# Kernel optimization log

Measured on AMD Instinct MI355X. Metric: run time of the kernel, lower is better.

Reference implementation:

```python
import jax, jax.numpy as jnp
import numpy as np

SLOPE = 0.2  # leaky_relu_slope for both LVC block and kernel predictor (passed through)
DILATIONS = (1, 3, 9, 27)
HOP = 256
STRIDE = 8
IN_CH = 32
KSZ = 3  # conv_kernel_size


def conv1d(x, w, b, dilation=1, padding=0):
    # x: (B,C,T), w: (O,I,K) torch layout
    y = jax.lax.conv_general_dilated(
        x, w, window_strides=(1,), padding=[(padding, padding)],
        rhs_dilation=(dilation,), dimension_numbers=('NCH', 'OIH', 'NCH'))
    return y + b[None, :, None]


def conv_transpose1d(x, w, b, stride, padding, output_padding=0):
    # w: torch ConvTranspose1d layout (Cin, Cout, K)
    w_ = jnp.flip(w, -1).transpose(1, 0, 2)  # (Cout, Cin, K)
    K = w.shape[2]
    pad = (K - 1 - padding, K - 1 - padding + output_padding)
    y = jax.lax.conv_general_dilated(
        x, w_, window_strides=(1,), padding=[pad],
        lhs_dilation=(stride,), dimension_numbers=('NCH', 'OIH', 'NCH'))
    return y + b[None, :, None]


def lrelu(x, slope=SLOPE):
    return jnp.where(x >= 0, x, slope * x)


def location_variable_convolution(x, kernel, bias, hop):
    # x: (B,C,T), kernel: (B,C,O,k,L), bias: (B,O,L); T == L*hop; dilation==1 path
    B, C, T = x.shape
    _, _, O, k, L = kernel.shape
    pad = (k - 1) // 2
    xp = jnp.pad(x, ((0, 0), (0, 0), (pad, pad)))
    # gather per-segment sliding windows: (L, hop, k) index into time axis
    idx = (jnp.arange(L)[:, None, None] * hop
           + jnp.arange(hop)[None, :, None]
           + jnp.arange(k)[None, None, :])
    xw = xp[:, :, idx]  # (B, C, L, hop, k)
    o = jnp.einsum('bclsk,bcokl->bols', xw, kernel)  # (B, O, L, hop)
    o = o + bias[:, :, :, None]
    return o.reshape(B, O, L * hop)


def kernel_predictor(spec, kp_in_w, kp_in_b, rb_w1, rb_b1, rb_w2, rb_b2,
                     kern_w, kern_b, bias_w, bias_b):
    B, _, L = spec.shape
    h = conv1d(spec, kp_in_w, kp_in_b, padding=2)  # k=5, pad=2
    for i in range(3):  # num_blocks = 3
        r = h
        h = conv1d(h, rb_w1[i], rb_b1[i], padding=1)
        h = lrelu(h)
        h = conv1d(h, rb_w2[i], rb_b2[i], padding=1)
        h = lrelu(h) + r
    kh = conv1d(h, kern_w, kern_b, padding=1)
    bh = conv1d(h, bias_w, bias_b, padding=1)
    n_layers = len(DILATIONS)
    kernels = kh.reshape(B, n_layers, IN_CH, 2 * IN_CH, KSZ, L)
    biases = bh.reshape(B, n_layers, 2 * IN_CH, L)
    return kernels, biases


def reference(hidden_states, spectrogram, convt_w, convt_b, kp_in_w, kp_in_b,
              rb_w1, rb_b1, rb_w2, rb_b2, kern_w, kern_b, bias_w, bias_b,
              lvc_w, lvc_b):
    h = conv_transpose1d(hidden_states, convt_w, convt_b,
                         stride=STRIDE, padding=STRIDE // 2 + STRIDE % 2,
                         output_padding=STRIDE % 2)
    kernels, biases = kernel_predictor(spectrogram, kp_in_w, kp_in_b,
                                       rb_w1, rb_b1, rb_w2, rb_b2,
                                       kern_w, kern_b, bias_w, bias_b)
    for i, d in enumerate(DILATIONS):
        r = h
        h = lrelu(h)
        h = conv1d(h, lvc_w[i], lvc_b[i], dilation=d, padding=d * (KSZ - 1) // 2)
        h = lrelu(h)
        h = location_variable_convolution(h, kernels[:, i], biases[:, i], HOP)
        h = jax.nn.sigmoid(h[:, :IN_CH, :]) * jnp.tanh(h[:, IN_CH:, :]) + r
    return h


def setup_inputs() -> dict:
    key = jax.random.key(0)
    ks = jax.random.split(key, 12)
    B, COND, L, H = 4, 100, 256, 64
    T = L * HOP  # 65536 output samples
    s = jnp.float32(0.02)
    d = {}
    d['hidden_states'] = jax.random.normal(ks[0], (B, IN_CH, T // STRIDE), jnp.float32)
    d['spectrogram'] = jax.random.normal(ks[1], (B, COND, L), jnp.float32)
    d['convt_w'] = jax.random.normal(ks[2], (IN_CH, IN_CH, 2 * STRIDE), jnp.float32) * s
    d['convt_b'] = jnp.zeros((IN_CH,), jnp.float32)
    d['kp_in_w'] = jax.random.normal(ks[3], (H, COND, 5), jnp.float32) * s
    d['kp_in_b'] = jnp.zeros((H,), jnp.float32)
    d['rb_w1'] = jax.random.normal(ks[4], (3, H, H, 3), jnp.float32) * s
    d['rb_b1'] = jnp.zeros((3, H), jnp.float32)
    d['rb_w2'] = jax.random.normal(ks[5], (3, H, H, 3), jnp.float32) * s
    d['rb_b2'] = jnp.zeros((3, H), jnp.float32)
    KC = IN_CH * 2 * IN_CH * KSZ * len(DILATIONS)  # 24576
    d['kern_w'] = jax.random.normal(ks[6], (KC, H, 3), jnp.float32) * s
    d['kern_b'] = jnp.zeros((KC,), jnp.float32)
    BC = 2 * IN_CH * len(DILATIONS)  # 256
    d['bias_w'] = jax.random.normal(ks[7], (BC, H, 3), jnp.float32) * s
    d['bias_b'] = jnp.zeros((BC,), jnp.float32)
    d['lvc_w'] = jax.random.normal(ks[8], (len(DILATIONS), IN_CH, IN_CH, 3), jnp.float32) * s
    d['lvc_b'] = jnp.zeros((len(DILATIONS), IN_CH), jnp.float32)
    return d
```

## Files before the change

kernel.cpp:

```cpp
#include <hip/hip_runtime.h>
#include <math.h>

#define NB 4
#define T 65536
#define TIN 8192
#define LL 256
#define KCL 6144

__device__ __forceinline__ float lrelu_f(float v) { return v >= 0.f ? v : 0.2f * v; }

__global__ void __launch_bounds__(256) prep1(
    const float* __restrict__ rb_w1, const float* __restrict__ rb_w2,
    const float* __restrict__ kp_in_w,
    float* __restrict__ trb, float* __restrict__ tkpin) {
  __shared__ float t[64][193];
  const int bid = blockIdx.x, tid = threadIdx.x;
  if (bid < 6) {
    int i = bid >> 1, which = bid & 1;
    const float* src = (which ? rb_w2 : rb_w1) + (size_t)i * 12288;
    float* dst = trb + (size_t)bid * 12288;
    for (int idx = tid; idx < 64 * 192; idx += 256) {
      int o = idx / 192, J = idx % 192;
      t[o][J] = src[(size_t)o * 192 + J];
    }
    __syncthreads();
    for (int idx = tid; idx < 64 * 192; idx += 256) {
      int J = idx >> 6, o = idx & 63;
      dst[(size_t)J * 64 + o] = t[o][J];
    }
  } else {
    for (int idx = tid; idx < 500 * 64; idx += 256) {
      int row = idx >> 6, o = idx & 63;
      tkpin[idx] = kp_in_w[o * 500 + row];
    }
  }
}

union Phase1LDS {
  struct { float xs[32][264]; float wm[64][128]; } cvt;
  struct { float hs[4][64][20]; float xsp[4][100][24]; } trk;
};

__global__ void __launch_bounds__(512) phase1(
    const float* __restrict__ x, const float* __restrict__ cw,
    const float* __restrict__ cbias, float* __restrict__ hout,
    const float* __restrict__ spec,
    const float* __restrict__ tkpin, const float* __restrict__ kp_in_b,
    const float* __restrict__ trb, const float* __restrict__ rb_b1,
    const float* __restrict__ rb_b2, float* __restrict__ kp_h) {
  __shared__ Phase1LDS sm;
  const int bid = blockIdx.x;
  const int tid = threadIdx.x;
  const int lane = tid & 63, wv = tid >> 6;

  if (bid < 64) {
    if (wv >= 4) return;
    const int unit = bid * 4 + wv;
    const int b = unit >> 6;
    const int chunk = unit & 63;
    const int l0 = chunk * 4;
    const int og = lane >> 1;
    const int colg = lane & 1;
    const int colg8 = colg * 8;
    const int obase = og * 2;
    float (*hsu)[20] = sm.trk.hs[wv];
    float (*xspu)[24] = sm.trk.xsp[wv];

    for (int i = lane; i < 64 * 20; i += 64) ((float*)hsu)[i] = 0.f;

    for (int i = lane; i < 100 * 24; i += 64) {
      int cin = i / 24, cx = i - cin * 24;
      float v = 0.f;
      if (cx < 20) {
        int labs = l0 - 8 + cx;
        if (labs >= 0 && labs < 256)
          v = spec[((size_t)b * 100 + cin) * LL + labs];
      }
      xspu[cin][cx] = v;
    }

    float hcur[2][8];
    {
      float acc[2][8];
      float2 bb = *(const float2*)(kp_in_b + obase);
#pragma unroll
      for (int q = 0; q < 8; ++q) { acc[0][q] = bb.x; acc[1][q] = bb.y; }
#pragma unroll 2
      for (int cin = 0; cin < 100; ++cin) {
        float x12[12];
        *(float4*)&x12[0] = *(const float4*)&xspu[cin][colg8];
        *(float4*)&x12[4] = *(const float4*)&xspu[cin][colg8 + 4];
        *(float4*)&x12[8] = *(const float4*)&xspu[cin][colg8 + 8];
        const float* wp = tkpin + (size_t)(cin * 5) * 64 + obase;
#pragma unroll
        for (int k = 0; k < 5; ++k) {
          float2 w = *(const float2*)(wp + k * 64);
#pragma unroll
          for (int q = 0; q < 8; ++q) {
            acc[0][q] += x12[q + k] * w.x;
            acc[1][q] += x12[q + k] * w.y;
          }
        }
      }
#pragma unroll
      for (int oi = 0; oi < 2; ++oi)
#pragma unroll
        for (int q = 0; q < 8; ++q) {
          int rel = colg8 + q, labs = l0 - 6 + rel;
          float v = (labs >= 0 && labs < 256) ? acc[oi][q] : 0.f;
          hcur[oi][q] = v;
          hsu[obase + oi][rel + 1] = v;
        }
    }

    for (int cv = 0; cv < 6; ++cv) {
      const float* wb = trb + (size_t)cv * 12288;
      const float* bp = (cv & 1) ? rb_b2 + (cv >> 1) * 64 : rb_b1 + (cv >> 1) * 64;
      float2 bb = *(const float2*)(bp + obase);
      float acc[2][8];
#pragma unroll
      for (int q = 0; q < 8; ++q) { acc[0][q] = bb.x; acc[1][q] = bb.y; }
#pragma unroll 2
      for (int c = 0; c < 64; ++c) {
        float x10[10];
        *(float4*)&x10[0] = *(const float4*)&hsu[c][colg8];
        *(float4*)&x10[4] = *(const float4*)&hsu[c][colg8 + 4];
        *(float2*)&x10[8] = *(const float2*)&hsu[c][colg8 + 8];
        const float* wp = wb + (size_t)(c * 192) + obase;
        float2 w0 = *(const float2*)(wp);
        float2 w1 = *(const float2*)(wp + 64);
        float2 w2 = *(const float2*)(wp + 128);
#pragma unroll
        for (int q = 0; q < 8; ++q) {
          acc[0][q] += x10[q] * w0.x + x10[q + 1] * w1.x + x10[q + 2] * w2.x;
          acc[1][q] += x10[q] * w0.y + x10[q + 1] * w1.y + x10[q + 2] * w2.y;
        }
      }
      const int lo = cv + 1, hi = 15 - cv;
#pragma unroll
      for (int oi = 0; oi < 2; ++oi)
#pragma unroll
        for (int q = 0; q < 8; ++q) {
          int rel = colg8 + q, labs = l0 - 6 + rel;
          float v = lrelu_f(acc[oi][q]);
          if (cv & 1) v += hcur[oi][q];
          bool ok = (rel >= lo) && (rel < hi) && (labs >= 0) && (labs < 256);
          v = ok ? v : 0.f;
          if (cv & 1) hcur[oi][q] = v;
          if (cv < 5) hsu[obase + oi][rel + 1] = v;
        }
    }

#pragma unroll
    for (int oi = 0; oi < 2; ++oi)
#pragma unroll
      for (int q = 0; q < 8; ++q) {
        int rel = colg8 + q;
        if (rel >= 6 && rel < 10)
          kp_h[((size_t)b * 64 + obase + oi) * LL + l0 + rel - 6] = hcur[oi][q];
      }
    return;
  }

  const int cb = bid - 64;
  const int bx = cb % 33;
  const int rr = cb / 33;
  const int mtp = rr & 1;
  const int b = rr >> 1;
  const int s0base = bx * 256;
  float (*xs)[264] = sm.cvt.xs;
  float (*wm)[128] = sm.cvt.wm;

  const float* xb = x + (size_t)b * 32 * TIN;
  for (int idx = tid; idx < 32 * 64; idx += 512) {
    int c = idx >> 6, q = idx & 63;
    int p = s0base + q * 4;
    float4 v = (p + 3 < TIN) ? *(const float4*)(xb + c * TIN + p)
                             : make_float4(0.f, 0.f, 0.f, 0.f);
    *(float4*)&xs[c][4 + 4 * q] = v;
  }
  if (tid < 32) {
    int p = s0base - 1;
    xs[tid][3] = (p >= 0) ? xb[tid * TIN + p] : 0.f;
  }
  for (int idx = tid; idx < 8192; idx += 512) {
    int i = idx >> 7, mm = idx & 127;
    int oo = mtp * 16 + (mm >> 3), k0 = mm & 7;
    wm[i][mm] = (i < 32) ? cw[i * 512 + oo * 16 + k0]
                         : cw[(i - 32) * 512 + oo * 16 + k0 + 8];
  }
  __syncthreads();

  float acc[2][8][4];
#pragma unroll
  for (int ol = 0; ol < 2; ++ol) {
    float bo = cbias[mtp * 16 + wv * 2 + ol];
#pragma unroll
    for (int k0 = 0; k0 < 8; ++k0)
#pragma unroll
      for (int si = 0; si < 4; ++si) acc[ol][k0][si] = bo;
  }

  for (int c = 0; c < 32; ++c) {
    float xm1[4], x0[4];
#pragma unroll
    for (int si = 0; si < 4; ++si) {
      xm1[si] = xs[c][lane + si * 64 + 3];
      x0[si]  = xs[c][lane + si * 64 + 4];
    }
    float w0[16], w1[16];
#pragma unroll
    for (int q = 0; q < 4; ++q) {
      *(float4*)&w0[q * 4] = *(const float4*)&wm[c][wv * 16 + q * 4];
      *(float4*)&w1[q * 4] = *(const float4*)&wm[32 + c][wv * 16 + q * 4];
    }
#pragma unroll
    for (int ol = 0; ol < 2; ++ol)
#pragma unroll
      for (int k0 = 0; k0 < 8; ++k0)
#pragma unroll
        for (int si = 0; si < 4; ++si)
          acc[ol][k0][si] += x0[si] * w0[ol * 8 + k0] + xm1[si] * w1[ol * 8 + k0];
  }

#pragma unroll
  for (int ol = 0; ol < 2; ++ol) {
    float* ob = hout + ((size_t)b * 32 + mtp * 16 + wv * 2 + ol) * T;
#pragma unroll
    for (int si = 0; si < 4; ++si) {
      int tb = (s0base + lane + si * 64) * 8 - 4;
      if (tb >= 0 && tb < T)
        *(float4*)(ob + tb) = make_float4(acc[ol][0][si], acc[ol][1][si],
                                          acc[ol][2][si], acc[ol][3][si]);
      if (tb + 4 >= 0 && tb + 4 < T)
        *(float4*)(ob + tb + 4) = make_float4(acc[ol][4][si], acc[ol][5][si],
                                              acc[ol][6][si], acc[ol][7][si]);
    }
  }
}

__global__ void __launch_bounds__(256, 3) kern_head(const float* __restrict__ kp_h,
                                                    const float* __restrict__ kw,
                                                    const float* __restrict__ kb,
                                                    const float* __restrict__ bias_w,
                                                    const float* __restrict__ bias_b,
                                                    float* __restrict__ kh,
                                                    float* __restrict__ bh, int layer) {
    const int bx = blockIdx.x, b = blockIdx.y;
    const bool isbias = (bx >= 192);
    const int tid = threadIdx.x, lane = tid & 63, wv = tid >> 6;
    __shared__ float xs[32][264];
    __shared__ float ws[96][36];

    int g = 0, oc0 = 0, ci = 0, kk = 0, ocb0 = 0;
    const float* wsrc;
    size_t wrow0;
    int wstride;
    if (!isbias) {
        g = bx >> 1; oc0 = (bx & 1) * 32;
        ci = g / 3; kk = g - ci * 3;
        wsrc = kw + (size_t)layer * KCL * 192;
        wrow0 = (size_t)((ci * 64 + oc0) * 3 + kk) * 192;
        wstride = 576;
    } else {
        ocb0 = (bx - 192) * 32;
        wsrc = bias_w;
        wrow0 = (size_t)ocb0 * 192;
        wstride = 192;
    }

    float acc[8][4];
#pragma unroll
    for (int oi = 0; oi < 8; ++oi) {
        float bv = isbias ? bias_b[ocb0 + wv * 8 + oi]
                          : kb[layer * KCL + (ci * 64 + oc0 + wv * 8 + oi) * 3 + kk];
#pragma unroll
        for (int si = 0; si < 4; ++si) acc[oi][si] = bv;
    }

    for (int half = 0; half < 2; ++half) {
        const int hc0 = half * 32;
        __syncthreads();
        for (int idx = tid; idx < 32 * 64; idx += 256) {
            int c = idx >> 6, q = idx & 63;
            *(float4*)&xs[c][4 + 4 * q] =
                *(const float4*)(kp_h + ((size_t)b * 64 + hc0 + c) * LL + 4 * q);
        }
        if (tid < 32) { xs[tid][3] = 0.f; xs[tid][260] = 0.f; }
        for (int idx = tid; idx < 3072; idx += 256) {
            int ocl = idx / 96, jj = idx - ocl * 96;
            ws[jj][ocl] = wsrc[wrow0 + (size_t)ocl * wstride + hc0 * 3 + jj];
        }
        __syncthreads();
        for (int c = 0; c < 32; ++c) {
#pragma unroll
            for (int t = 0; t < 3; ++t) {
                float wv8[8];
                *(float4*)&wv8[0] = *(const float4*)&ws[c * 3 + t][wv * 8];
                *(float4*)&wv8[4] = *(const float4*)&ws[c * 3 + t][wv * 8 + 4];
                float xv[4];
#pragma unroll
                for (int si = 0; si < 4; ++si) xv[si] = xs[c][lane + si * 64 + t + 3];
#pragma unroll
                for (int oi = 0; oi < 8; ++oi)
#pragma unroll
                    for (int si = 0; si < 4; ++si)
                        acc[oi][si] += wv8[oi] * xv[si];
            }
        }
    }

    if (!isbias) {
#pragma unroll
        for (int si = 0; si < 4; ++si) {
            int l = lane + si * 64;
            float* op = kh + ((size_t)b * LL + l) * KCL + g * 64 + oc0 + wv * 8;
            *(float4*)(op)     = make_float4(acc[0][si], acc[1][si], acc[2][si], acc[3][si]);
            *(float4*)(op + 4) = make_float4(acc[4][si], acc[5][si], acc[6][si], acc[7][si]);
        }
    } else {
#pragma unroll
        for (int oi = 0; oi < 8; ++oi) {
            float* op = bh + ((size_t)b * 256 + ocb0 + wv * 8 + oi) * LL;
#pragma unroll
            for (int si = 0; si < 4; ++si)
                op[lane + si * 64] = acc[oi][si];
        }
    }
}

__global__ void __launch_bounds__(512, 4) layer_fused(
    const float* __restrict__ kh, const float* __restrict__ bh,
    const float* __restrict__ w, const float* __restrict__ bias,
    const float* __restrict__ hin, float* __restrict__ hout,
    int layer, int dil) {
    const int l = blockIdx.x, b = blockIdx.y;
    const int tid = threadIdx.x, lane = tid & 63, wv = tid >> 6;
    const int t0 = l * 256;
    __shared__ float xh[32][316];
    __shared__ float ks[KCL];
    __shared__ float ws[96][36];

    const float* hb = hin + (size_t)b * 32 * T;
    for (int idx = tid; idx < 32 * 64; idx += 512) {
        int c = idx >> 6, q = idx & 63;
        float4 v = *(const float4*)(hb + (size_t)c * T + t0 + 4 * q);
        *(float4*)&xh[c][32 + 4 * q] = make_float4(lrelu_f(v.x), lrelu_f(v.y),
                                                   lrelu_f(v.z), lrelu_f(v.w));
    }
    for (int idx = tid; idx < 32 * 60; idx += 512) {
        int c = idx / 60, r = idx - c * 60;
        int jj = (r < 32) ? r : (256 + r);
        int t = t0 + jj - 32;
        xh[c][jj] = (t >= 0 && t < T) ? lrelu_f(hb[(size_t)c * T + t]) : 0.f;
    }
    {
        const float4* kp = (const float4*)(kh + ((size_t)b * LL + l) * KCL);
        float4* kd = (float4*)ks;
        for (int idx = tid; idx < KCL / 4; idx += 512) kd[idx] = kp[idx];
    }
    for (int idx = tid; idx < 3072; idx += 512) {
        int oc = idx / 96, ck = idx - oc * 96;
        ws[ck][oc] = w[oc * 96 + ck];
    }
    __syncthreads();

    const int oc4 = wv * 4;
    float yv[5][4];
    {
        float a[5][4];
#pragma unroll
        for (int oi = 0; oi < 4; ++oi) {
            float bv = bias[oc4 + oi];
#pragma unroll
            for (int si = 0; si < 5; ++si) a[si][oi] = bv;
        }
        for (int c = 0; c < 32; ++c) {
#pragma unroll
            for (int k = 0; k < 3; ++k) {
                float4 wq = *(const float4*)&ws[c * 3 + k][oc4];
                float xv[5];
#pragma unroll
                for (int si = 0; si < 5; ++si) {
                    int col = lane + si * 64;
                    int colc = (col < 258) ? col : 257;
                    xv[si] = xh[c][colc + 31 + (k - 1) * dil];
                }
#pragma unroll
                for (int si = 0; si < 5; ++si) {
                    a[si][0] += xv[si] * wq.x;
                    a[si][1] += xv[si] * wq.y;
                    a[si][2] += xv[si] * wq.z;
                    a[si][3] += xv[si] * wq.w;
                }
            }
        }
#pragma unroll
        for (int si = 0; si < 5; ++si) {
            int t = t0 - 1 + lane + si * 64;
            bool tval = (t >= 0 && t < T);
#pragma unroll
            for (int oi = 0; oi < 4; ++oi)
                yv[si][oi] = tval ? lrelu_f(a[si][oi]) : 0.f;
        }
    }
    __syncthreads();

#pragma unroll
    for (int si = 0; si < 5; ++si) {
        int col = lane + si * 64;
        if (col < 258) {
#pragma unroll
            for (int oi = 0; oi < 4; ++oi) xh[oc4 + oi][col + 31] = yv[si][oi];
        }
    }
    __syncthreads();

    const int oc8 = (wv & 3) * 8;
    const int sh  = wv >> 2;
    float acc_a[8][2], acc_g[8][2];
#pragma unroll
    for (int oi = 0; oi < 8; ++oi) {
        float ba = bh[((size_t)b * 256 + layer * 64 + oc8 + oi) * LL + l];
        float bg = bh[((size_t)b * 256 + layer * 64 + 32 + oc8 + oi) * LL + l];
#pragma unroll
        for (int si = 0; si < 2; ++si) { acc_a[oi][si] = ba; acc_g[oi][si] = bg; }
    }

    for (int c = 0; c < 32; ++c) {
#pragma unroll
        for (int k = 0; k < 3; ++k) {
            const float* kr = ks + (c * 3 + k) * 64;
            float wa[8], wg[8];
            *(float4*)&wa[0] = *(const float4*)(kr + oc8);
            *(float4*)&wa[4] = *(const float4*)(kr + oc8 + 4);
            *(float4*)&wg[0] = *(const float4*)(kr + 32 + oc8);
            *(float4*)&wg[4] = *(const float4*)(kr + 32 + oc8 + 4);
            float xv2[2];
#pragma unroll
            for (int si = 0; si < 2; ++si) {
                int s = lane + (sh * 2 + si) * 64;
                xv2[si] = xh[c][s + k + 31];
            }
#pragma unroll
            for (int oi = 0; oi < 8; ++oi)
#pragma unroll
                for (int si = 0; si < 2; ++si) {
                    acc_a[oi][si] += wa[oi] * xv2[si];
                    acc_g[oi][si] += wg[oi] * xv2[si];
                }
        }
    }

#pragma unroll
    for (int oi = 0; oi < 8; ++oi) {
        const float* hip = hin + ((size_t)b * 32 + oc8 + oi) * T + t0;
        float* hop = hout + ((size_t)b * 32 + oc8 + oi) * T + t0;
#pragma unroll
        for (int si = 0; si < 2; ++si) {
            int s = lane + (sh * 2 + si) * 64;
            float a = acc_a[oi][si], g = acc_g[oi][si];
            float sg = 1.f / (1.f + __expf(-a));
            float th = tanhf(g);
            hop[s] = sg * th + hip[s];
        }
    }
}

extern "C" void kernel_launch(void* const* d_in, const int* in_sizes, int n_in,
                              void* d_out, int out_size, void* d_ws, size_t ws_size,
                              hipStream_t stream) {
    const float* hidden  = (const float*)d_in[0];
    const float* spec    = (const float*)d_in[1];
    const float* convt_w = (const float*)d_in[2];
    const float* convt_b = (const float*)d_in[3];
    const float* kp_in_w = (const float*)d_in[4];
    const float* kp_in_b = (const float*)d_in[5];
    const float* rb_w1   = (const float*)d_in[6];
    const float* rb_b1   = (const float*)d_in[7];
    const float* rb_w2   = (const float*)d_in[8];
    const float* rb_b2   = (const float*)d_in[9];
    const float* kern_w  = (const float*)d_in[10];
    const float* kern_b  = (const float*)d_in[11];
    const float* bias_w  = (const float*)d_in[12];
    const float* bias_b  = (const float*)d_in[13];
    const float* lvc_w   = (const float*)d_in[14];
    const float* lvc_b   = (const float*)d_in[15];

    float* wsp = (float*)d_ws;
    float* h_ws     = wsp;
    float* kh_layer = h_ws + (size_t)NB * 32 * T;
    float* bh       = kh_layer + (size_t)NB * LL * KCL;
    float* kp_h     = bh + (size_t)NB * 256 * LL;
    float* trb      = kp_h + (size_t)NB * 64 * LL;
    float* tkpin    = trb + (size_t)6 * 192 * 64;

    float* h0 = (float*)d_out;
    float* h1 = h_ws;

    prep1<<<dim3(7), 256, 0, stream>>>(rb_w1, rb_w2, kp_in_w, trb, tkpin);

    phase1<<<dim3(328), 512, 0, stream>>>(hidden, convt_w, convt_b, h0,
                                          spec, tkpin, kp_in_b,
                                          trb, rb_b1, rb_b2, kp_h);

    static const int dil[4] = {1, 3, 9, 27};
    float* hin = h0;
    float* hout = h1;
    for (int layer = 0; layer < 4; ++layer) {
        kern_head<<<dim3(layer == 0 ? 200 : 192, NB), 256, 0, stream>>>(
            kp_h, kern_w, kern_b, bias_w, bias_b, kh_layer, bh, layer);
        layer_fused<<<dim3(LL, NB), 512, 0, stream>>>(
            kh_layer, bh, lvc_w + (size_t)layer * 32 * 32 * 3, lvc_b + layer * 32,
            hin, hout, layer, dil[layer]);
        float* tmp = hin; hin = hout; hout = tmp;
    }
}
```

Measured before the change: 781.4 us.

## Pre-transpose weights into global scratch and drop LDS staging in head and LVC kernels

Adds a prep_kern pass per layer that transposes the kernel-predictor head weights, and has prep1 also transpose bias_w and lvc_w. kern_head and layer_fused then read weights directly from global memory in a coalesced layout instead of staging them in LDS; layer_fused also stops copying the per-segment kernel into shared memory and switches to 8 outputs by 3 columns per thread. The predictor part of phase1 now packs 8 waves per block that share one spectrogram tile, the unroll factor goes up, and kern_head occupancy goes from 3 to 4. The cost is an extra launch and about 4.7 MB of weight transposition per layer, plus more global or L2 weight traffic in the inner loops.

New measurement: 1.164 ms. 1.49x slower.

```diff
diff --git a/kernel.cpp b/kernel.cpp
--- a/kernel.cpp
+++ b/kernel.cpp
@@ -10,15 +10,24 @@
 __device__ __forceinline__ float lrelu_f(float v) { return v >= 0.f ? v : 0.2f * v; }
 
 __global__ void __launch_bounds__(256) prep1(
-    const float* __restrict__ rb_w1, const float* __restrict__ rb_w2,
-    const float* __restrict__ kp_in_w,
-    float* __restrict__ trb, float* __restrict__ tkpin) {
+    const float* __restrict__ bias_w, const float* __restrict__ rb_w1,
+    const float* __restrict__ rb_w2, const float* __restrict__ kp_in_w,
+    const float* __restrict__ lvc_w,
+    float* __restrict__ tbw, float* __restrict__ trb, float* __restrict__ tkpin,
+    float* __restrict__ tlvc) {
   __shared__ float t[64][193];
   const int bid = blockIdx.x, tid = threadIdx.x;
-  if (bid < 6) {
-    int i = bid >> 1, which = bid & 1;
-    const float* src = (which ? rb_w2 : rb_w1) + (size_t)i * 12288;
-    float* dst = trb + (size_t)bid * 12288;
+  if (bid < 10) {
+    const float* src; float* dst; int dstride, dcol;
+    if (bid < 6) {
+      int i = bid >> 1, which = bid & 1;
+      src = (which ? rb_w2 : rb_w1) + (size_t)i * 12288;
+      dst = trb + (size_t)bid * 12288; dstride = 64; dcol = 0;
+    } else {
+      int ob = bid - 6;
+      src = bias_w + (size_t)ob * 64 * 192;
+      dst = tbw; dstride = 256; dcol = ob * 64;
+    }
     for (int idx = tid; idx < 64 * 192; idx += 256) {
       int o = idx / 192, J = idx % 192;
       t[o][J] = src[(size_t)o * 192 + J];
@@ -26,19 +35,42 @@
     __syncthreads();
     for (int idx = tid; idx < 64 * 192; idx += 256) {
       int J = idx >> 6, o = idx & 63;
-      dst[(size_t)J * 64 + o] = t[o][J];
-    }
-  } else {
+      dst[(size_t)J * dstride + dcol + o] = t[o][J];
+    }
+  } else if (bid == 10) {
     for (int idx = tid; idx < 500 * 64; idx += 256) {
       int row = idx >> 6, o = idx & 63;
       tkpin[idx] = kp_in_w[o * 500 + row];
     }
+  } else {
+    for (int idx = tid; idx < 12288; idx += 256) {
+      int layer = idx / 3072, r = idx % 3072, ck = r >> 5, o = r & 31;
+      tlvc[idx] = lvc_w[(size_t)layer * 3072 + o * 96 + ck];
+    }
+  }
+}
+
+__global__ void __launch_bounds__(256) prep_kern(const float* __restrict__ kern_w,
+                                                 float* __restrict__ tkwL, int layer) {
+  __shared__ float t[64][193];
+  const int g = blockIdx.x, tid = threadIdx.x;
+  const int ci = g / 3, kk = g % 3;
+  const float* src = kern_w + ((size_t)layer * KCL + ci * 192 + kk) * 192;
+  float* dst = tkwL + (size_t)g * 12288;
+  for (int idx = tid; idx < 64 * 192; idx += 256) {
+    int o = idx / 192, J = idx % 192;
+    t[o][J] = src[(size_t)o * 576 + J];
+  }
+  __syncthreads();
+  for (int idx = tid; idx < 64 * 192; idx += 256) {
+    int J = idx >> 6, o = idx & 63;
+    dst[(size_t)J * 64 + o] = t[o][J];
   }
 }
 
 union Phase1LDS {
   struct { float xs[32][264]; float wm[64][128]; } cvt;
-  struct { float hs[4][64][20]; float xsp[4][100][24]; } trk;
+  struct { float hs[8][64][20]; float xsp[100][52]; } trk;
 };
 
 __global__ void __launch_bounds__(512) phase1(
@@ -53,31 +85,25 @@
   const int tid = threadIdx.x;
   const int lane = tid & 63, wv = tid >> 6;
 
-  if (bid < 64) {
-    if (wv >= 4) return;
-    const int unit = bid * 4 + wv;
-    const int b = unit >> 6;
-    const int chunk = unit & 63;
-    const int l0 = chunk * 4;
+  if (bid < 32) {
+    const int b = bid >> 3;
+    const int lb = (bid & 7) * 32;
+    const int l0 = lb + wv * 4;
     const int og = lane >> 1;
     const int colg = lane & 1;
     const int colg8 = colg * 8;
     const int obase = og * 2;
     float (*hsu)[20] = sm.trk.hs[wv];
-    float (*xspu)[24] = sm.trk.xsp[wv];
-
-    for (int i = lane; i < 64 * 20; i += 64) ((float*)hsu)[i] = 0.f;
-
-    for (int i = lane; i < 100 * 24; i += 64) {
-      int cin = i / 24, cx = i - cin * 24;
-      float v = 0.f;
-      if (cx < 20) {
-        int labs = l0 - 8 + cx;
-        if (labs >= 0 && labs < 256)
-          v = spec[((size_t)b * 100 + cin) * LL + labs];
-      }
-      xspu[cin][cx] = v;
-    }
+
+    for (int i = tid; i < 8 * 64 * 20; i += 512) ((float*)sm.trk.hs)[i] = 0.f;
+    for (int i = tid; i < 100 * 52; i += 512) {
+      int cin = i / 52, cx = i - cin * 52;
+      int labs = lb - 8 + cx;
+      float v = (labs >= 0 && labs < 256)
+                    ? spec[((size_t)b * 100 + cin) * LL + labs] : 0.f;
+      sm.trk.xsp[cin][cx] = v;
+    }
+    __syncthreads();
 
     float hcur[2][8];
     {
@@ -87,10 +113,11 @@
       for (int q = 0; q < 8; ++q) { acc[0][q] = bb.x; acc[1][q] = bb.y; }
 #pragma unroll 2
       for (int cin = 0; cin < 100; ++cin) {
+        const float* xrow = &sm.trk.xsp[cin][wv * 4 + colg8];
         float x12[12];
-        *(float4*)&x12[0] = *(const float4*)&xspu[cin][colg8];
-        *(float4*)&x12[4] = *(const float4*)&xspu[cin][colg8 + 4];
-        *(float4*)&x12[8] = *(const float4*)&xspu[cin][colg8 + 8];
+        *(float4*)&x12[0] = *(const float4*)(xrow);
+        *(float4*)&x12[4] = *(const float4*)(xrow + 4);
+        *(float4*)&x12[8] = *(const float4*)(xrow + 8);
         const float* wp = tkpin + (size_t)(cin * 5) * 64 + obase;
 #pragma unroll
         for (int k = 0; k < 5; ++k) {
@@ -120,7 +147,7 @@
       float acc[2][8];
 #pragma unroll
       for (int q = 0; q < 8; ++q) { acc[0][q] = bb.x; acc[1][q] = bb.y; }
-#pragma unroll 2
+#pragma unroll 4
       for (int c = 0; c < 64; ++c) {
         float x10[10];
         *(float4*)&x10[0] = *(const float4*)&hsu[c][colg8];
@@ -162,7 +189,7 @@
     return;
   }
 
-  const int cb = bid - 64;
+  const int cb = bid - 32;
   const int bx = cb % 33;
   const int rr = cb / 33;
   const int mtp = rr & 1;
@@ -239,280 +266,272 @@
   }
 }
 
-__global__ void __launch_bounds__(256, 3) kern_head(const float* __restrict__ kp_h,
-                                                    const float* __restrict__ kw,
+__global__ void __launch_bounds__(256, 4) kern_head(const float* __restrict__ kp_h,
+                                                    const float* __restrict__ tkwL,
                                                     const float* __restrict__ kb,
-                                                    const float* __restrict__ bias_w,
+                                                    const float* __restrict__ tbw,
                                                     const float* __restrict__ bias_b,
                                                     float* __restrict__ kh,
                                                     float* __restrict__ bh, int layer) {
-    const int bx = blockIdx.x, b = blockIdx.y;
-    const bool isbias = (bx >= 192);
-    const int tid = threadIdx.x, lane = tid & 63, wv = tid >> 6;
-    __shared__ float xs[32][264];
-    __shared__ float ws[96][36];
-
-    int g = 0, oc0 = 0, ci = 0, kk = 0, ocb0 = 0;
-    const float* wsrc;
-    size_t wrow0;
-    int wstride;
-    if (!isbias) {
-        g = bx >> 1; oc0 = (bx & 1) * 32;
-        ci = g / 3; kk = g - ci * 3;
-        wsrc = kw + (size_t)layer * KCL * 192;
-        wrow0 = (size_t)((ci * 64 + oc0) * 3 + kk) * 192;
-        wstride = 576;
-    } else {
-        ocb0 = (bx - 192) * 32;
-        wsrc = bias_w;
-        wrow0 = (size_t)ocb0 * 192;
-        wstride = 192;
-    }
-
-    float acc[8][4];
+  const int bx = blockIdx.x, b = blockIdx.y;
+  const bool isbias = (bx >= 192);
+  const int tid = threadIdx.x, lane = tid & 63, wv = tid >> 6;
+  __shared__ float xs[32][264];
+
+  int g = 0, oc0 = 0, ci = 0, kk = 0, ocb0 = 0;
+  const float* wbase;
+  int wstride;
+  if (!isbias) {
+    g = bx >> 1; oc0 = (bx & 1) * 32;
+    ci = g / 3; kk = g - ci * 3;
+    wbase = tkwL + (size_t)g * 12288 + oc0 + wv * 8;
+    wstride = 64;
+  } else {
+    ocb0 = (bx - 192) * 32;
+    wbase = tbw + ocb0 + wv * 8;
+    wstride = 256;
+  }
+
+  float acc[8][4];
+#pragma unroll
+  for (int oi = 0; oi < 8; ++oi) {
+    float bv = isbias ? bias_b[ocb0 + wv * 8 + oi]
+                      : kb[layer * KCL + (ci * 64 + oc0 + wv * 8 + oi) * 3 + kk];
+#pragma unroll
+    for (int si = 0; si < 4; ++si) acc[oi][si] = bv;
+  }
+
+  for (int half = 0; half < 2; ++half) {
+    const int hc0 = half * 32;
+    __syncthreads();
+    for (int idx = tid; idx < 32 * 64; idx += 256) {
+      int c = idx >> 6, q = idx & 63;
+      *(float4*)&xs[c][4 + 4 * q] =
+          *(const float4*)(kp_h + ((size_t)b * 64 + hc0 + c) * LL + 4 * q);
+    }
+    if (tid < 32) { xs[tid][3] = 0.f; xs[tid][260] = 0.f; }
+    __syncthreads();
+    const float* wb2 = wbase + (size_t)(hc0 * 3) * wstride;
+    for (int c = 0; c < 32; ++c) {
+#pragma unroll
+      for (int t = 0; t < 3; ++t) {
+        float w8[8];
+        *(float4*)&w8[0] = *(const float4*)(wb2 + (size_t)(c * 3 + t) * wstride);
+        *(float4*)&w8[4] = *(const float4*)(wb2 + (size_t)(c * 3 + t) * wstride + 4);
+        float xv[4];
+#pragma unroll
+        for (int si = 0; si < 4; ++si) xv[si] = xs[c][lane + si * 64 + t + 3];
+#pragma unroll
+        for (int oi = 0; oi < 8; ++oi)
+#pragma unroll
+          for (int si = 0; si < 4; ++si)
+            acc[oi][si] += w8[oi] * xv[si];
+      }
+    }
+  }
+
+  if (!isbias) {
+#pragma unroll
+    for (int si = 0; si < 4; ++si) {
+      int l = lane + si * 64;
+      float* op = kh + ((size_t)b * LL + l) * KCL + g * 64 + oc0 + wv * 8;
+      *(float4*)(op)     = make_float4(acc[0][si], acc[1][si], acc[2][si], acc[3][si]);
+      *(float4*)(op + 4) = make_float4(acc[4][si], acc[5][si], acc[6][si], acc[7][si]);
+    }
+  } else {
 #pragma unroll
     for (int oi = 0; oi < 8; ++oi) {
-        float bv = isbias ? bias_b[ocb0 + wv * 8 + oi]
-                          : kb[layer * KCL + (ci * 64 + oc0 + wv * 8 + oi) * 3 + kk];
-#pragma unroll
-        for (int si = 0; si < 4; ++si) acc[oi][si] = bv;
-    }
-
-    for (int half = 0; half < 2; ++half) {
-        const int hc0 = half * 32;
-        __syncthreads();
-        for (int idx = tid; idx < 32 * 64; idx += 256) {
-            int c = idx >> 6, q = idx & 63;
-            *(float4*)&xs[c][4 + 4 * q] =
-                *(const float4*)(kp_h + ((size_t)b * 64 + hc0 + c) * LL + 4 * q);
-        }
-        if (tid < 32) { xs[tid][3] = 0.f; xs[tid][260] = 0.f; }
-        for (int idx = tid; idx < 3072; idx += 256) {
-            int ocl = idx / 96, jj = idx - ocl * 96;
-            ws[jj][ocl] = wsrc[wrow0 + (size_t)ocl * wstride + hc0 * 3 + jj];
-        }
-        __syncthreads();
-        for (int c = 0; c < 32; ++c) {
-#pragma unroll
-            for (int t = 0; t < 3; ++t) {
-                float wv8[8];
-                *(float4*)&wv8[0] = *(const float4*)&ws[c * 3 + t][wv * 8];
-                *(float4*)&wv8[4] = *(const float4*)&ws[c * 3 + t][wv * 8 + 4];
-                float xv[4];
-#pragma unroll
-                for (int si = 0; si < 4; ++si) xv[si] = xs[c][lane + si * 64 + t + 3];
-#pragma unroll
-                for (int oi = 0; oi < 8; ++oi)
-#pragma unroll
-                    for (int si = 0; si < 4; ++si)
-                        acc[oi][si] += wv8[oi] * xv[si];
-            }
-        }
-    }
-
-    if (!isbias) {
-#pragma unroll
-        for (int si = 0; si < 4; ++si) {
-            int l = lane + si * 64;
-            float* op = kh + ((size_t)b * LL + l) * KCL + g * 64 + oc0 + wv * 8;
-            *(float4*)(op)     = make_float4(acc[0][si], acc[1][si], acc[2][si], acc[3][si]);
-            *(float4*)(op + 4) = make_float4(acc[4][si], acc[5][si], acc[6][si], acc[7][si]);
-        }
-    } else {
-#pragma unroll
-        for (int oi = 0; oi < 8; ++oi) {
-            float* op = bh + ((size_t)b * 256 + ocb0 + wv * 8 + oi) * LL;
-#pragma unroll
-            for (int si = 0; si < 4; ++si)
-                op[lane + si * 64] = acc[oi][si];
-        }
-    }
+      float* op = bh + ((size_t)b * 256 + ocb0 + wv * 8 + oi) * LL;
+#pragma unroll
+      for (int si = 0; si < 4; ++si)
+        op[lane + si * 64] = acc[oi][si];
+    }
+  }
 }
 
 __global__ void __launch_bounds__(512, 4) layer_fused(
     const float* __restrict__ kh, const float* __restrict__ bh,
-    const float* __restrict__ w, const float* __restrict__ bias,
+    const float* __restrict__ wT, const float* __restrict__ bias,
     const float* __restrict__ hin, float* __restrict__ hout,
     int layer, int dil) {
-    const int l = blockIdx.x, b = blockIdx.y;
-    const int tid = threadIdx.x, lane = tid & 63, wv = tid >> 6;
-    const int t0 = l * 256;
-    __shared__ float xh[32][316];
-    __shared__ float ks[KCL];
-    __shared__ float ws[96][36];
-
-    const float* hb = hin + (size_t)b * 32 * T;
-    for (int idx = tid; idx < 32 * 64; idx += 512) {
-        int c = idx >> 6, q = idx & 63;
-        float4 v = *(const float4*)(hb + (size_t)c * T + t0 + 4 * q);
-        *(float4*)&xh[c][32 + 4 * q] = make_float4(lrelu_f(v.x), lrelu_f(v.y),
-                                                   lrelu_f(v.z), lrelu_f(v.w));
-    }
-    for (int idx = tid; idx < 32 * 60; idx += 512) {
-        int c = idx / 60, r = idx - c * 60;
-        int jj = (r < 32) ? r : (256 + r);
-        int t = t0 + jj - 32;
-        xh[c][jj] = (t >= 0 && t < T) ? lrelu_f(hb[(size_t)c * T + t]) : 0.f;
-    }
-    {
-        const float4* kp = (const float4*)(kh + ((size_t)b * LL + l) * KCL);
-        float4* kd = (float4*)ks;
-        for (int idx = tid; idx < KCL / 4; idx += 512) kd[idx] = kp[idx];
-    }
-    for (int idx = tid; idx < 3072; idx += 512) {
-        int oc = idx / 96, ck = idx - oc * 96;
-        ws[ck][oc] = w[oc * 96 + ck];
-    }
-    __syncthreads();
-
-    const int oc4 = wv * 4;
-    float yv[5][4];
-    {
-        float a[5][4];
-#pragma unroll
-        for (int oi = 0; oi < 4; ++oi) {
-            float bv = bias[oc4 + oi];
-#pragma unroll
-            for (int si = 0; si < 5; ++si) a[si][oi] = bv;
+  const int l = blockIdx.x, b = blockIdx.y;
+  const int tid = threadIdx.x, lane = tid & 63, wv = tid >> 6;
+  const int t0 = l * 256;
+  __shared__ float xh[32][316];
+
+  const float* hb = hin + (size_t)b * 32 * T;
+  for (int idx = tid; idx < 32 * 64; idx += 512) {
+    int c = idx >> 6, q = idx & 63;
+    float4 v = *(const float4*)(hb + (size_t)c * T + t0 + 4 * q);
+    *(float4*)&xh[c][32 + 4 * q] = make_float4(lrelu_f(v.x), lrelu_f(v.y),
+                                               lrelu_f(v.z), lrelu_f(v.w));
+  }
+  for (int idx = tid; idx < 32 * 60; idx += 512) {
+    int c = idx / 60, r = idx - c * 60;
+    int jj = (r < 32) ? r : (256 + r);
+    int t = t0 + jj - 32;
+    xh[c][jj] = (t >= 0 && t < T) ? lrelu_f(hb[(size_t)c * T + t]) : 0.f;
+  }
+  __syncthreads();
+
+  const int oc8b = (wv & 3) * 8;
+  const int hw = wv >> 2;
+  float yv[3][8];
+  {
+    float a[3][8];
+    float bv8[8];
+    *(float4*)&bv8[0] = *(const float4*)(bias + oc8b);
+    *(float4*)&bv8[4] = *(const float4*)(bias + oc8b + 4);
+#pragma unroll
+    for (int si = 0; si < 3; ++si)
+#pragma unroll
+      for (int oi = 0; oi < 8; ++oi) a[si][oi] = bv8[oi];
+    for (int c = 0; c < 32; ++c) {
+#pragma unroll
+      for (int k = 0; k < 3; ++k) {
+        const float* wp = wT + (size_t)(c * 3 + k) * 32 + oc8b;
+        float w8[8];
+        *(float4*)&w8[0] = *(const float4*)(wp);
+        *(float4*)&w8[4] = *(const float4*)(wp + 4);
+        float xv[3];
+#pragma unroll
+        for (int si = 0; si < 3; ++si) {
+          int col = lane + (si * 2 + hw) * 64;
+          int colc = (col < 258) ? col : 257;
+          xv[si] = xh[c][colc + 31 + (k - 1) * dil];
         }
-        for (int c = 0; c < 32; ++c) {
-#pragma unroll
-            for (int k = 0; k < 3; ++k) {
-                float4 wq = *(const float4*)&ws[c * 3 + k][oc4];
-                float xv[5];
-#pragma unroll
-                for (int si = 0; si < 5; ++si) {
-                    int col = lane + si * 64;
-                    int colc = (col < 258) ? col : 257;
-                    xv[si] = xh[c][colc + 31 + (k - 1) * dil];
-                }
-#pragma unroll
-                for (int si = 0; si < 5; ++si) {
-                    a[si][0] += xv[si] * wq.x;
-                    a[si][1] += xv[si] * wq.y;
-                    a[si][2] += xv[si] * wq.z;
-                    a[si][3] += xv[si] * wq.w;
-                }
-            }
+#pragma unroll
+        for (int si = 0; si < 3; ++si)
+#pragma unroll
+          for (int oi = 0; oi < 8; ++oi)
+            a[si][oi] += xv[si] * w8[oi];
+      }
+    }
+#pragma unroll
+    for (int si = 0; si < 3; ++si) {
+      int col = lane + (si * 2 + hw) * 64;
+      int t = t0 - 1 + col;
+      bool tval = (t >= 0 && t < T) && (col < 258);
+#pragma unroll
+      for (int oi = 0; oi < 8; ++oi)
+        yv[si][oi] = tval ? lrelu_f(a[si][oi]) : 0.f;
+    }
+  }
+  __syncthreads();
+
+#pragma unroll
+  for (int si = 0; si < 3; ++si) {
+    int col = lane + (si * 2 + hw) * 64;
+    if (col < 258) {
+#pragma unroll
+      for (int oi = 0; oi < 8; ++oi) xh[oc8b + oi][col + 31] = yv[si][oi];
+    }
+  }
+  __syncthreads();
+
+  const int oc8 = (wv & 3) * 8;
+  const int sh  = wv >> 2;
+  const float* krb = kh + ((size_t)b * LL + l) * KCL;
+  float acc_a[8][2], acc_g[8][2];
+#pragma unroll
+  for (int oi = 0; oi < 8; ++oi) {
+    float ba = bh[((size_t)b * 256 + layer * 64 + oc8 + oi) * LL + l];
+    float bg = bh[((size_t)b * 256 + layer * 64 + 32 + oc8 + oi) * LL + l];
+#pragma unroll
+    for (int si = 0; si < 2; ++si) { acc_a[oi][si] = ba; acc_g[oi][si] = bg; }
+  }
+
+  for (int c = 0; c < 32; ++c) {
+#pragma unroll
+    for (int k = 0; k < 3; ++k) {
+      const float* kr = krb + (size_t)(c * 3 + k) * 64;
+      float wa[8], wg[8];
+      *(float4*)&wa[0] = *(const float4*)(kr + oc8);
+      *(float4*)&wa[4] = *(const float4*)(kr + oc8 + 4);
+      *(float4*)&wg[0] = *(const float4*)(kr + 32 + oc8);
+      *(float4*)&wg[4] = *(const float4*)(kr + 32 + oc8 + 4);
+      float xv2[2];
+#pragma unroll
+      for (int si = 0; si < 2; ++si) {
+        int s = lane + (sh * 2 + si) * 64;
+        xv2[si] = xh[c][s + k + 31];
+      }
+#pragma unroll
+      for (int oi = 0; oi < 8; ++oi)
+#pragma unroll
+        for (int si = 0; si < 2; ++si) {
+          acc_a[oi][si] += wa[oi] * xv2[si];
+          acc_g[oi][si] += wg[oi] * xv2[si];
         }
-#pragma unroll
-        for (int si = 0; si < 5; ++si) {
-            int t = t0 - 1 + lane + si * 64;
-            bool tval = (t >= 0 && t < T);
-#pragma unroll
-            for (int oi = 0; oi < 4; ++oi)
-                yv[si][oi] = tval ? lrelu_f(a[si][oi]) : 0.f;
-        }
-    }
-    __syncthreads();
-
-#pragma unroll
-    for (int si = 0; si < 5; ++si) {
-        int col = lane + si * 64;
-        if (col < 258) {
-#pragma unroll
-            for (int oi = 0; oi < 4; ++oi) xh[oc4 + oi][col + 31] = yv[si][oi];
-        }
-    }
-    __syncthreads();
-
-    const int oc8 = (wv & 3) * 8;
-    const int sh  = wv >> 2;
-    float acc_a[8][2], acc_g[8][2];
-#pragma unroll
-    for (int oi = 0; oi < 8; ++oi) {
-        float ba = bh[((size_t)b * 256 + layer * 64 + oc8 + oi) * LL + l];
-        float bg = bh[((size_t)b * 256 + layer * 64 + 32 + oc8 + oi) * LL + l];
-#pragma unroll
-        for (int si = 0; si < 2; ++si) { acc_a[oi][si] = ba; acc_g[oi][si] = bg; }
-    }
-
-    for (int c = 0; c < 32; ++c) {
-#pragma unroll
-        for (int k = 0; k < 3; ++k) {
-            const float* kr = ks + (c * 3 + k) * 64;
-            float wa[8], wg[8];
-            *(float4*)&wa[0] = *(const float4*)(kr + oc8);
-            *(float4*)&wa[4] = *(const float4*)(kr + oc8 + 4);
-            *(float4*)&wg[0] = *(const float4*)(kr + 32 + oc8);
-            *(float4*)&wg[4] = *(const float4*)(kr + 32 + oc8 + 4);
-            float xv2[2];
-#pragma unroll
-            for (int si = 0; si < 2; ++si) {
-                int s = lane + (sh * 2 + si) * 64;
-                xv2[si] = xh[c][s + k + 31];
-            }
-#pragma unroll
-            for (int oi = 0; oi < 8; ++oi)
-#pragma unroll
-                for (int si = 0; si < 2; ++si) {
-                    acc_a[oi][si] += wa[oi] * xv2[si];
-                    acc_g[oi][si] += wg[oi] * xv2[si];
-                }
-        }
-    }
-
-#pragma unroll
-    for (int oi = 0; oi < 8; ++oi) {
-        const float* hip = hin + ((size_t)b * 32 + oc8 + oi) * T + t0;
-        float* hop = hout + ((size_t)b * 32 + oc8 + oi) * T + t0;
-#pragma unroll
-        for (int si = 0; si < 2; ++si) {
-            int s = lane + (sh * 2 + si) * 64;
-            float a = acc_a[oi][si], g = acc_g[oi][si];
-            float sg = 1.f / (1.f + __expf(-a));
-            float th = tanhf(g);
-            hop[s] = sg * th + hip[s];
-        }
-    }
+    }
+  }
+
+#pragma unroll
+  for (int oi = 0; oi < 8; ++oi) {
+    const float* hip = hin + ((size_t)b * 32 + oc8 + oi) * T + t0;
+    float* hop = hout + ((size_t)b * 32 + oc8 + oi) * T + t0;
+#pragma unroll
+    for (int si = 0; si < 2; ++si) {
+      int s = lane + (sh * 2 + si) * 64;
+      float a = acc_a[oi][si], g = acc_g[oi][si];
+      float sg = 1.f / (1.f + __expf(-a));
+      float th = tanhf(g);
+      hop[s] = sg * th + hip[s];
+    }
+  }
 }
 
 extern "C" void kernel_launch(void* const* d_in, const int* in_sizes, int n_in,
                               void* d_out, int out_size, void* d_ws, size_t ws_size,
                               hipStream_t stream) {
-    const float* hidden  = (const float*)d_in[0];
-    const float* spec    = (const float*)d_in[1];
-    const float* convt_w = (const float*)d_in[2];
-    const float* convt_b = (const float*)d_in[3];
-    const float* kp_in_w = (const float*)d_in[4];
-    const float* kp_in_b = (const float*)d_in[5];
-    const float* rb_w1   = (const float*)d_in[6];
-    const float* rb_b1   = (const float*)d_in[7];
-    const float* rb_w2   = (const float*)d_in[8];
-    const float* rb_b2   = (const float*)d_in[9];
-    const float* kern_w  = (const float*)d_in[10];
-    const float* kern_b  = (const float*)d_in[11];
-    const float* bias_w  = (const float*)d_in[12];
-    const float* bias_b  = (const float*)d_in[13];
-    const float* lvc_w   = (const float*)d_in[14];
-    const float* lvc_b   = (const float*)d_in[15];
-
-    float* wsp = (float*)d_ws;
-    float* h_ws     = wsp;
-    float* kh_layer = h_ws + (size_t)NB * 32 * T;
-    float* bh       = kh_layer + (size_t)NB * LL * KCL;
-    float* kp_h     = bh + (size_t)NB * 256 * LL;
-    float* trb      = kp_h + (size_t)NB * 64 * LL;
-    float* tkpin    = trb + (size_t)6 * 192 * 64;
-
-    float* h0 = (float*)d_out;
-    float* h1 = h_ws;
-
-    prep1<<<dim3(7), 256, 0, stream>>>(rb_w1, rb_w2, kp_in_w, trb, tkpin);
-
-    phase1<<<dim3(328), 512, 0, stream>>>(hidden, convt_w, convt_b, h0,
-                                          spec, tkpin, kp_in_b,
-                                          trb, rb_b1, rb_b2, kp_h);
-
-    static const int dil[4] = {1, 3, 9, 27};
-    float* hin = h0;
-    float* hout = h1;
-    for (int layer = 0; layer < 4; ++layer) {
-        kern_head<<<dim3(layer == 0 ? 200 : 192, NB), 256, 0, stream>>>(
-            kp_h, kern_w, kern_b, bias_w, bias_b, kh_layer, bh, layer);
-        layer_fused<<<dim3(LL, NB), 512, 0, stream>>>(
-            kh_layer, bh, lvc_w + (size_t)layer * 32 * 32 * 3, lvc_b + layer * 32,
-            hin, hout, layer, dil[layer]);
-        float* tmp = hin; hin = hout; hout = tmp;
-    }
+  const float* hidden  = (const float*)d_in[0];
+  const float* spec    = (const float*)d_in[1];
+  const float* convt_w = (const float*)d_in[2];
+  const float* convt_b = (const float*)d_in[3];
+  const float* kp_in_w = (const float*)d_in[4];
+  const float* kp_in_b = (const float*)d_in[5];
+  const float* rb_w1   = (const float*)d_in[6];
+  const float* rb_b1   = (const float*)d_in[7];
+  const float* rb_w2   = (const float*)d_in[8];
+  const float* rb_b2   = (const float*)d_in[9];
+  const float* kern_w  = (const float*)d_in[10];
+  const float* kern_b  = (const float*)d_in[11];
+  const float* bias_w  = (const float*)d_in[12];
+  const float* bias_b  = (const float*)d_in[13];
+  const float* lvc_w   = (const float*)d_in[14];
+  const float* lvc_b   = (const float*)d_in[15];
+
+  float* wsp = (float*)d_ws;
+  float* h_ws     = wsp;
+  float* kh_layer = h_ws + (size_t)NB * 32 * T;
+  float* bh       = kh_layer + (size_t)NB * LL * KCL;
+  float* kp_h     = bh + (size_t)NB * 256 * LL;
+  float* tkwL     = kp_h + (size_t)NB * 64 * LL;
+  float* tbw      = tkwL + (size_t)96 * 192 * 64;
+  float* trb      = tbw + (size_t)192 * 256;
+  float* tkpin    = trb + (size_t)6 * 192 * 64;
+  float* tlvc     = tkpin + (size_t)500 * 64;
+
+  float* h0 = (float*)d_out;
+  float* h1 = h_ws;
+
+  prep1<<<dim3(12), 256, 0, stream>>>(bias_w, rb_w1, rb_w2, kp_in_w, lvc_w,
+                                      tbw, trb, tkpin, tlvc);
+
+  phase1<<<dim3(296), 512, 0, stream>>>(hidden, convt_w, convt_b, h0,
+                                        spec, tkpin, kp_in_b,
+                                        trb, rb_b1, rb_b2, kp_h);
+
+  static const int dil[4] = {1, 3, 9, 27};
+  float* hin = h0;
+  float* hout = h1;
+  for (int layer = 0; layer < 4; ++layer) {
+    prep_kern<<<dim3(96), 256, 0, stream>>>(kern_w, tkwL, layer);
+    kern_head<<<dim3(layer == 0 ? 200 : 192, NB), 256, 0, stream>>>(
+        kp_h, tkwL, kern_b, tbw, bias_b, kh_layer, bh, layer);
+    layer_fused<<<dim3(LL, NB), 512, 0, stream>>>(
+        kh_layer, bh, tlvc + (size_t)layer * 3072, lvc_b + layer * 32,
+        hin, hout, layer, dil[layer]);
+    float* tmp = hin; hin = hout; hout = tmp;
+  }
 }
```
